# Kernel tuning notes

Measured on AMD Instinct MI355X. Metric: run time of the kernel, lower is better.

## Reference

```python
import jax, jax.numpy as jnp
import numpy as np

B, IN_LEN, NN, IN_DIM = 32, 28, 2048, 1
E, ND = 256, 256          # embed_dim, node_dim
H = E + ND                # hidden_dim = 512
N_LAYERS = 3
OUT_LEN = 28


def setup_inputs() -> dict:
    key = jax.random.key(0)
    ks = jax.random.split(key, 16)
    x_node = jax.random.normal(ks[0], (B, IN_LEN, NN, IN_DIM), jnp.float32)
    # x_state channels: [0]=cumulative cases, [1]=infected I, [2]=population N
    col0 = jax.random.uniform(ks[1], (B, IN_LEN, NN, 1), jnp.float32) * 100.0
    colI = jax.random.uniform(ks[2], (B, IN_LEN, NN, 1), jnp.float32) * 100.0 + 1.0
    colN = 1e4 * (1.0 + 0.1 * jax.random.uniform(ks[3], (B, IN_LEN, NN, 1), jnp.float32))
    x_state = jnp.concatenate([col0, colI, colN], axis=-1)
    node_emb = jax.random.normal(ks[4], (NN, ND), jnp.float32) * 0.05
    W_ts = jax.random.normal(ks[5], (E, IN_DIM * IN_LEN), jnp.float32) * 0.05
    b_ts = jnp.zeros((E,), jnp.float32)
    enc_W1 = jax.random.normal(ks[6], (N_LAYERS, H, H), jnp.float32) * 0.02
    enc_b1 = jnp.zeros((N_LAYERS, H), jnp.float32)
    enc_W2 = jax.random.normal(ks[7], (N_LAYERS, H, H), jnp.float32) * 0.02
    enc_b2 = jnp.zeros((N_LAYERS, H), jnp.float32)
    Wb = jax.random.normal(ks[8], (1, H), jnp.float32) * 0.05
    bb = jnp.zeros((1,), jnp.float32)
    Wg = jax.random.normal(ks[9], (1, H), jnp.float32) * 0.05
    bg = jnp.zeros((1,), jnp.float32)
    return dict(x_node=x_node, x_state=x_state, node_emb=node_emb,
                W_ts=W_ts, b_ts=b_ts, enc_W1=enc_W1, enc_b1=enc_b1,
                enc_W2=enc_W2, enc_b2=enc_b2, Wb=Wb, bb=bb, Wg=Wg, bg=bg)


def _forward(x_node, x_state, node_emb, W_ts, b_ts,
             enc_W1, enc_b1, enc_W2, enc_b2, Wb, bb, Wg, bg):
    Bn, Lh, Nn, _ = x_node.shape
    # [B,L,N,D] -> [B,N,L*D] (channel = in_dim*in_len for 1x1 conv == linear)
    flat = jnp.transpose(x_node[..., :IN_DIM], (0, 2, 1, 3)).reshape(Bn, Nn, Lh * IN_DIM)
    ts = flat @ W_ts.T + b_ts                                  # [B,N,E]
    h = jnp.concatenate(
        [ts, jnp.broadcast_to(node_emb[None], (Bn,) + node_emb.shape)], axis=-1)  # [B,N,H]
    for l in range(enc_W1.shape[0]):                            # residual MLP encoder
        z = jnp.maximum(h @ enc_W1[l].T + enc_b1[l], 0.0)
        h = h + z @ enc_W2[l].T + enc_b2[l]
    b = jax.nn.sigmoid(h @ Wb.T + bb)                           # [B,N,1] infection rate
    g = jax.nn.sigmoid(h @ Wg.T + bg)                           # [B,N,1] recovery rate

    Npop = x_state[:, -1, :, 2:3]                               # [B,N,1]
    I_hist = x_state[..., 1:2] / g[:, None]                     # [B,L,N,1]
    Iin_hist = jnp.maximum(
        I_hist[:, 1:] - I_hist[:, :-1] + x_state[:, :-1, :, 1:2], 0.0)  # [B,L-1,N,1]
    t1 = jnp.arange(Lh - 1, 0, -1, dtype=jnp.float32)
    w1 = jnp.exp(-g[:, None] * t1[None, :, None, None])         # [B,L-1,N,1]
    I_Tm1 = jnp.sum(w1 * Iin_hist, axis=1)                      # [B,N,1]
    R_Tm1 = Npop - x_state[:, -2, :, 0:1]
    S_Tm1 = Npop - I_Tm1 - R_Tm1
    Iin0 = b * S_Tm1 * I_Tm1 / Npop
    Rin0 = g * I_hist[:, -1, :, 0:1]
    Iin_hist = jnp.concatenate([Iin_hist, Iin0[:, None]], axis=1)  # [B,L,N,1]
    S = S_Tm1 - Iin0
    t2 = jnp.arange(Lh, 0, -1, dtype=jnp.float32)
    w2 = jnp.exp(-g[:, None] * t2[None, :, None, None])
    I = jnp.sum(w2 * Iin_hist, axis=1)                          # [B,N,1]
    R = R_Tm1 + Rin0

    # The torch loop recomputes sum_i exp(-g*(L-i))*Iin_i each step; exact identity:
    # I_new = exp(-g) * (I_old + Iin_new). O(T) scan instead of O(T^2).
    decay = jnp.exp(-g)

    def step(carry, _):
        S, I, R = carry
        Iin = b * S * I / Npop
        S = S - Iin
        Rin = g * I            # uses pre-update I_T, matching torch order
        I = decay * (I + Iin)
        R = R + Rin
        return (S, I, R), Rin

    _, rins = jax.lax.scan(step, (S, I, R), None, length=OUT_LEN)  # [T,B,N,1]
    return jnp.transpose(rins, (1, 0, 2, 3))                       # [B,out_len,N,1]


def reference(x_node, x_state, node_emb, W_ts, b_ts, enc_W1, enc_b1,
              enc_W2, enc_b2, Wb, bb, Wg, bg):
    return _forward(x_node, x_state, node_emb, W_ts, b_ts,
                    enc_W1, enc_b1, enc_W2, enc_b2, Wb, bb, Wg, bg)
```

## Files before the change

kernel.cpp:

```cpp
#include <hip/hip_runtime.h>
#include <hip/hip_bf16.h>
#include <math.h>

#define BATCH 32
#define IN_LEN 28
#define NN 2048
#define E 256
#define H 512
#define N_LAYERS 3
#define OUT_LEN 28
#define M_ROWS (BATCH * NN)

typedef unsigned short u16;
typedef unsigned int   u32;
typedef __attribute__((ext_vector_type(8))) short short8;
typedef __attribute__((ext_vector_type(4))) float f32x4;

__device__ __forceinline__ u16 f2h(float x) {
    union { _Float16 h; u16 u; } v; v.h = (_Float16)x; return v.u;
}
__device__ __forceinline__ float h2f(u16 u) {
    union { _Float16 h; u16 u; } v; v.u = u; return (float)v.h;
}

__device__ __forceinline__ void gload_lds16(const void* g, void* l) {
    __builtin_amdgcn_global_load_lds(
        (const __attribute__((address_space(1))) void*)g,
        (__attribute__((address_space(3))) void*)l, 16, 0, 0);
}

__global__ __launch_bounds__(256)
void k_split2(const float* __restrict__ w1, const float* __restrict__ w2,
              u16* __restrict__ hi, u16* __restrict__ lo, int nW)
{
    int i = blockIdx.x * 256 + threadIdx.x;
    float v = (i < nW) ? w1[i] : w2[i - nW];
    u16 h = f2h(v);
    hi[i] = h;
    lo[i] = f2h(v - h2f(h));
}

__global__ __launch_bounds__(256)
void k_ts(const float* __restrict__ x_node, const float* __restrict__ node_emb,
          const float* __restrict__ W_ts, const float* __restrict__ b_ts,
          u16* __restrict__ hhi, u16* __restrict__ hlo)
{
    __shared__ float xs[IN_LEN][64];
    const int tid = threadIdx.x;
    const int b   = blockIdx.y;
    const int n0  = blockIdx.x * 64;

    for (int idx = tid; idx < IN_LEN * 64; idx += 256) {
        int l = idx >> 6, i = idx & 63;
        xs[l][i] = x_node[((size_t)b * IN_LEN + l) * NN + n0 + i];
    }
    __syncthreads();

    float w[IN_LEN];
    #pragma unroll
    for (int j = 0; j < IN_LEN; j++) w[j] = W_ts[tid * IN_LEN + j];
    const float bias = b_ts[tid];

    for (int i = 0; i < 64; i++) {
        float acc = bias;
        #pragma unroll
        for (int j = 0; j < IN_LEN; j++) acc += xs[j][i] * w[j];
        size_t row = (size_t)b * NN + n0 + i;
        u16 thi = f2h(acc);
        hhi[row * H + tid] = thi;
        hlo[row * H + tid] = f2h(acc - h2f(thi));
        float ev = node_emb[(size_t)(n0 + i) * 256 + tid];
        u16 ehi = f2h(ev);
        hhi[row * H + E + tid] = ehi;
        hlo[row * H + E + tid] = f2h(ev - h2f(ehi));
    }
}

__global__ __launch_bounds__(256)
void k_gemm1(const u16* __restrict__ Ahi, const u16* __restrict__ Alo,
             const u16* __restrict__ Whi, const u16* __restrict__ Wlo,
             const float* __restrict__ bias, u16* __restrict__ Z)
{
    __shared__ __align__(16) u16 smem[32768];

    const int tid = threadIdx.x;
    const int ln  = tid & 63;
    const int wv  = tid >> 6;

    const int id   = blockIdx.x;
    const int c    = (id >> 3) & 3;
    const int r    = (id & 7) | ((id >> 5) << 3);
    const int row0 = r * 128;
    const int col0 = c * 128;

    const int rbase = (wv & 1) * 64;
    const int cbase = (wv >> 1) * 64;

    const int lr = ln >> 2;
    const int lc = ln & 3;

    const u16* sgsrc; int sofs; int tb;
    if      (wv == 0) { sgsrc = Ahi; sofs = 0;     tb = row0; }
    else if (wv == 1) { sgsrc = Alo; sofs = 8192;  tb = row0; }
    else if (wv == 2) { sgsrc = Whi; sofs = 16384; tb = col0; }
    else              { sgsrc = Wlo; sofs = 24576; tb = col0; }

    auto stage = [&](int p, int kt) {
        u16* dstbuf = smem + sofs + p * 4096;
        #pragma unroll
        for (int i = 0; i < 8; i++) {
            int row = i * 16 + lr;
            int sc  = lc ^ ((row >> 1) & 3);
            gload_lds16(sgsrc + (size_t)(tb + row) * H + kt + sc * 8,
                        dstbuf + i * 512);
        }
    };

    f32x4 acc[4][4];
    #pragma unroll
    for (int m = 0; m < 4; m++)
        #pragma unroll
        for (int n = 0; n < 4; n++) acc[m][n] = (f32x4)(0.f);

    stage(0, 0);

    const int wl = ln & 15;

    for (int t = 0; t < 16; t++) {
        const int p = t & 1;
        __syncthreads();
        if (t + 1 < 16) stage(1 - p, (t + 1) * 32);

        const u16* bAh = smem + 0     + p * 4096;
        const u16* bAl = smem + 8192  + p * 4096;
        const u16* bWh = smem + 16384 + p * 4096;
        const u16* bWl = smem + 24576 + p * 4096;

        short8 ahi[4], alo[4], whi[4], wlo[4];
        #pragma unroll
        for (int m = 0; m < 4; m++) {
            int rr = rbase + m * 16 + wl;
            int cc = ((ln >> 4) ^ ((rr >> 1) & 3)) * 8;
            ahi[m] = *(const short8*)&bAh[rr * 32 + cc];
            alo[m] = *(const short8*)&bAl[rr * 32 + cc];
        }
        #pragma unroll
        for (int n = 0; n < 4; n++) {
            int wr = cbase + n * 16 + wl;
            int cc = ((ln >> 4) ^ ((wr >> 1) & 3)) * 8;
            whi[n] = *(const short8*)&bWh[wr * 32 + cc];
            wlo[n] = *(const short8*)&bWl[wr * 32 + cc];
        }
        #pragma unroll
        for (int m = 0; m < 4; m++)
            #pragma unroll
            for (int n = 0; n < 4; n++) {
                acc[m][n] = __builtin_amdgcn_mfma_f32_16x16x32_f16(ahi[m], whi[n], acc[m][n], 0, 0, 0);
                acc[m][n] = __builtin_amdgcn_mfma_f32_16x16x32_f16(ahi[m], wlo[n], acc[m][n], 0, 0, 0);
                acc[m][n] = __builtin_amdgcn_mfma_f32_16x16x32_f16(alo[m], whi[n], acc[m][n], 0, 0, 0);
            }
    }

    __syncthreads();
    u16* zb = smem + wv * 4096;
    float bv[4];
    #pragma unroll
    for (int n = 0; n < 4; n++) bv[n] = bias[col0 + cbase + n * 16 + wl];
    #pragma unroll
    for (int m = 0; m < 4; m++)
        #pragma unroll
        for (int n = 0; n < 4; n++)
            #pragma unroll
            for (int rg = 0; rg < 4; rg++) {
                int row_l = m * 16 + (ln >> 4) * 4 + rg;
                zb[row_l * 64 + n * 16 + wl] =
                    f2h(fmaxf(acc[m][n][rg] + bv[n], 0.f));
            }
    const int cr = ln >> 3;
    const int cc = (ln & 7) * 8;
    #pragma unroll
    for (int p2 = 0; p2 < 8; p2++) {
        int row_l = cr + p2 * 8;
        uint4 v = *(const uint4*)&zb[row_l * 64 + cc];
        *(uint4*)&Z[(size_t)(row0 + rbase + row_l) * H + col0 + cbase + cc] = v;
    }
}

__global__ __launch_bounds__(256)
void k_gemm2(const u16* __restrict__ Z,
             const u16* __restrict__ Whi, const u16* __restrict__ Wlo,
             const float* __restrict__ bias,
             u16* HHi, u16* HLo)
{
    __shared__ __align__(16) u16 smem[24576];

    const int tid = threadIdx.x;
    const int ln  = tid & 63;
    const int wv  = tid >> 6;

    const int id   = blockIdx.x;
    const int c    = (id >> 3) & 3;
    const int r    = (id & 7) | ((id >> 5) << 3);
    const int row0 = r * 128;
    const int col0 = c * 128;

    const int rbase = (wv & 1) * 64;
    const int cbase = (wv >> 1) * 64;

    const int lr = ln >> 2;
    const int lc = ln & 3;

    const u16* sgsrc; int sofs; int tb; int iofs; int niss;
    if      (wv == 0) { sgsrc = Z;   sofs = 0;     tb = row0;      iofs = 0;    niss = 4; }
    else if (wv == 3) { sgsrc = Z;   sofs = 0;     tb = row0 + 64; iofs = 2048; niss = 4; }
    else if (wv == 1) { sgsrc = Whi; sofs = 8192;  tb = col0;      iofs = 0;    niss = 8; }
    else              { sgsrc = Wlo; sofs = 16384; tb = col0;      iofs = 0;    niss = 8; }

    auto stage = [&](int p, int kt) {
        u16* dstbuf = smem + sofs + p * 4096 + iofs;
        #pragma unroll
        for (int i = 0; i < 8; i++) {
            if (i >= niss) break;
            int row = i * 16 + lr;
            int sc  = lc ^ ((row >> 1) & 3);
            gload_lds16(sgsrc + (size_t)(tb + row) * H + kt + sc * 8,
                        dstbuf + i * 512);
        }
    };

    stage(0, 0);

    const int cr  = ln >> 3;
    const int ccl = (ln & 7) * 4;
    uint2 resh[2][8], resl[2][8];
    #pragma unroll
    for (int nh = 0; nh < 2; nh++) {
        const int gc0 = col0 + cbase + nh * 32 + ccl;
        #pragma unroll
        for (int p2 = 0; p2 < 8; p2++) {
            size_t gidx = (size_t)(row0 + rbase + cr + p2 * 8) * H + gc0;
            resh[nh][p2] = *(const uint2*)(HHi + gidx);
            resl[nh][p2] = *(const uint2*)(HLo + gidx);
        }
    }

    f32x4 acc[4][4];
    #pragma unroll
    for (int m = 0; m < 4; m++)
        #pragma unroll
        for (int n = 0; n < 4; n++) acc[m][n] = (f32x4)(0.f);

    const int wl = ln & 15;

    for (int t = 0; t < 16; t++) {
        const int p = t & 1;
        __syncthreads();
        if (t + 1 < 16) stage(1 - p, (t + 1) * 32);

        const u16* bZ  = smem + 0     + p * 4096;
        const u16* bWh = smem + 8192  + p * 4096;
        const u16* bWl = smem + 16384 + p * 4096;

        short8 az[4], whi[4], wlo[4];
        #pragma unroll
        for (int m = 0; m < 4; m++) {
            int rr = rbase + m * 16 + wl;
            int cc = ((ln >> 4) ^ ((rr >> 1) & 3)) * 8;
            az[m] = *(const short8*)&bZ[rr * 32 + cc];
        }
        #pragma unroll
        for (int n = 0; n < 4; n++) {
            int wr = cbase + n * 16 + wl;
            int cc = ((ln >> 4) ^ ((wr >> 1) & 3)) * 8;
            whi[n] = *(const short8*)&bWh[wr * 32 + cc];
            wlo[n] = *(const short8*)&bWl[wr * 32 + cc];
        }
        #pragma unroll
        for (int m = 0; m < 4; m++)
            #pragma unroll
            for (int n = 0; n < 4; n++) {
                acc[m][n] = __builtin_amdgcn_mfma_f32_16x16x32_f16(az[m], whi[n], acc[m][n], 0, 0, 0);
                acc[m][n] = __builtin_amdgcn_mfma_f32_16x16x32_f16(az[m], wlo[n], acc[m][n], 0, 0, 0);
            }
    }

    __syncthreads();
    float* fb = (float*)smem + wv * 2048;

    #pragma unroll
    for (int nh = 0; nh < 2; nh++) {
        #pragma unroll
        for (int m = 0; m < 4; m++)
            #pragma unroll
            for (int j = 0; j < 2; j++)
                #pragma unroll
                for (int rg = 0; rg < 4; rg++) {
                    int row_l = m * 16 + (ln >> 4) * 4 + rg;
                    fb[row_l * 32 + j * 16 + wl] = acc[m][nh * 2 + j][rg];
                }
        const int gc0 = col0 + cbase + nh * 32 + ccl;
        float4 bv = *(const float4*)&bias[gc0];
        #pragma unroll
        for (int p2 = 0; p2 < 8; p2++) {
            int row_l = cr + p2 * 8;
            size_t gidx = (size_t)(row0 + rbase + row_l) * H + gc0;
            uint2 uh = resh[nh][p2];
            uint2 ul = resl[nh][p2];
            float4 a = *(const float4*)&fb[row_l * 32 + ccl];
            float v0 = a.x + bv.x + h2f((u16)(uh.x & 0xFFFF)) + h2f((u16)(ul.x & 0xFFFF));
            float v1 = a.y + bv.y + h2f((u16)(uh.x >> 16))    + h2f((u16)(ul.x >> 16));
            float v2 = a.z + bv.z + h2f((u16)(uh.y & 0xFFFF)) + h2f((u16)(ul.y & 0xFFFF));
            float v3 = a.w + bv.w + h2f((u16)(uh.y >> 16))    + h2f((u16)(ul.y >> 16));
            u16 h0 = f2h(v0), h1 = f2h(v1), h2 = f2h(v2), h3 = f2h(v3);
            uint2 oh, ol;
            oh.x = (u32)h0 | ((u32)h1 << 16);
            oh.y = (u32)h2 | ((u32)h3 << 16);
            ol.x = (u32)f2h(v0 - h2f(h0)) | ((u32)f2h(v1 - h2f(h1)) << 16);
            ol.y = (u32)f2h(v2 - h2f(h2)) | ((u32)f2h(v3 - h2f(h3)) << 16);
            *(uint2*)(HHi + gidx) = oh;
            *(uint2*)(HLo + gidx) = ol;
        }
    }
}

__global__ __launch_bounds__(256)
void k_head(const u16* __restrict__ hhi, const u16* __restrict__ hlo,
            const float* __restrict__ Wb, const float* __restrict__ bb,
            const float* __restrict__ Wg, const float* __restrict__ bg,
            float* __restrict__ bArr, float* __restrict__ gArr)
{
    const int lane = threadIdx.x & 63;
    const int row  = blockIdx.x * 4 + (threadIdx.x >> 6);

    uint4 uh = *(const uint4*)(hhi + (size_t)row * H + lane * 8);
    uint4 ul = *(const uint4*)(hlo + (size_t)row * H + lane * 8);
    u32 ph[4] = {uh.x, uh.y, uh.z, uh.w};
    u32 pl[4] = {ul.x, ul.y, ul.z, ul.w};
    float hv[8];
    #pragma unroll
    for (int k = 0; k < 4; k++) {
        hv[2 * k]     = h2f((u16)(ph[k] & 0xFFFF)) + h2f((u16)(pl[k] & 0xFFFF));
        hv[2 * k + 1] = h2f((u16)(ph[k] >> 16))    + h2f((u16)(pl[k] >> 16));
    }
    float4 wb0 = *(const float4*)(Wb + lane * 8);
    float4 wb1 = *(const float4*)(Wb + lane * 8 + 4);
    float4 wg0 = *(const float4*)(Wg + lane * 8);
    float4 wg1 = *(const float4*)(Wg + lane * 8 + 4);

    float sb = hv[0] * wb0.x + hv[1] * wb0.y + hv[2] * wb0.z + hv[3] * wb0.w
             + hv[4] * wb1.x + hv[5] * wb1.y + hv[6] * wb1.z + hv[7] * wb1.w;
    float sg = hv[0] * wg0.x + hv[1] * wg0.y + hv[2] * wg0.z + hv[3] * wg0.w
             + hv[4] * wg1.x + hv[5] * wg1.y + hv[6] * wg1.z + hv[7] * wg1.w;

    #pragma unroll
    for (int off = 32; off >= 1; off >>= 1) {
        sb += __shfl_xor(sb, off);
        sg += __shfl_xor(sg, off);
    }
    if (lane == 0) {
        bArr[row] = 1.f / (1.f + expf(-(sb + bb[0])));
        gArr[row] = 1.f / (1.f + expf(-(sg + bg[0])));
    }
}

__global__ __launch_bounds__(256)
void k_sir(const float* __restrict__ x_state,
           const float* __restrict__ bArr, const float* __restrict__ gArr,
           float* __restrict__ out)
{
    const int row = blockIdx.x * 256 + threadIdx.x;
    const int bb_ = row / NN;
    const int n   = row % NN;

    const float g = gArr[row];
    const float b = bArr[row];
    const float d = expf(-g);

    const float* xs = x_state + ((size_t)bb_ * IN_LEN) * (NN * 3) + (size_t)n * 3;

    float x1_prev = xs[1];
    float Ih_prev = x1_prev / g;
    float acc = 0.f;
    #pragma unroll 4
    for (int t = 1; t <= IN_LEN - 1; ++t) {
        float x1 = xs[(size_t)t * (NN * 3) + 1];
        float Ih = x1 / g;
        float Iin = fmaxf(Ih - Ih_prev + x1_prev, 0.f);
        acc = acc * d + Iin;
        Ih_prev = Ih;
        x1_prev = x1;
    }
    float ITm1 = acc * d;
    float Npop = xs[(size_t)(IN_LEN - 1) * (NN * 3) + 2];
    float RTm1 = Npop - xs[(size_t)(IN_LEN - 2) * (NN * 3) + 0];
    float STm1 = Npop - ITm1 - RTm1;
    float Iin0 = b * STm1 * ITm1 / Npop;
    float S = STm1 - Iin0;
    float I = d * (ITm1 + Iin0);

    float* op = out + ((size_t)bb_ * OUT_LEN) * NN + n;
    #pragma unroll 4
    for (int k = 0; k < OUT_LEN; k++) {
        float Iin = b * S * I / Npop;
        S = S - Iin;
        float Rin = g * I;
        I = d * (I + Iin);
        op[(size_t)k * NN] = Rin;
    }
}

extern "C" void kernel_launch(void* const* d_in, const int* in_sizes, int n_in,
                              void* d_out, int out_size, void* d_ws, size_t ws_size,
                              hipStream_t stream)
{
    const float* x_node   = (const float*)d_in[0];
    const float* x_state  = (const float*)d_in[1];
    const float* node_emb = (const float*)d_in[2];
    const float* W_ts     = (const float*)d_in[3];
    const float* b_ts     = (const float*)d_in[4];
    const float* enc_W1   = (const float*)d_in[5];
    const float* enc_b1   = (const float*)d_in[6];
    const float* enc_W2   = (const float*)d_in[7];
    const float* enc_b2   = (const float*)d_in[8];
    const float* Wb       = (const float*)d_in[9];
    const float* bb       = (const float*)d_in[10];
    const float* Wg       = (const float*)d_in[11];
    const float* bg       = (const float*)d_in[12];
    float* out = (float*)d_out;

    u16* hhi   = (u16*)d_ws;
    u16* hlo   = hhi + (size_t)M_ROWS * H;
    u16* wHi   = hlo + (size_t)M_ROWS * H;
    u16* wLo   = wHi + (size_t)6 * H * H;
    float* bArr = (float*)(wLo + (size_t)6 * H * H);
    float* gArr = bArr + M_ROWS;
    u16* z     = (u16*)(gArr + M_ROWS);

    size_t used  = (size_t)((char*)z - (char*)d_ws);
    size_t avail = (ws_size > used) ? ws_size - used : 0;
    long long chunkLL = (long long)(avail / (H * sizeof(u16))) & ~1023LL;
    int chunk = (chunkLL > M_ROWS) ? M_ROWS : (int)chunkLL;
    if (chunk < 1024) chunk = 1024;

    const int nW = N_LAYERS * H * H;
    k_split2<<<2 * nW / 256, 256, 0, stream>>>(enc_W1, enc_W2, wHi, wLo, nW);

    k_ts<<<dim3(NN / 64, BATCH), 256, 0, stream>>>(x_node, node_emb, W_ts, b_ts, hhi, hlo);

    for (int l = 0; l < N_LAYERS; l++) {
        const u16* W1hi = wHi + (size_t)l * H * H;
        const u16* W1lo = wLo + (size_t)l * H * H;
        const u16* W2hi = wHi + (size_t)nW + (size_t)l * H * H;
        const u16* W2lo = wLo + (size_t)nW + (size_t)l * H * H;
        const float* b1 = enc_b1 + (size_t)l * H;
        const float* b2 = enc_b2 + (size_t)l * H;
        for (int r = 0; r < M_ROWS; r += chunk) {
            int rows = (M_ROWS - r < chunk) ? (M_ROWS - r) : chunk;
            u16* hrhi = hhi + (size_t)r * H;
            u16* hrlo = hlo + (size_t)r * H;
            int nblk = (rows / 128) * 4;
            k_gemm1<<<nblk, 256, 0, stream>>>(hrhi, hrlo, W1hi, W1lo, b1, z);
            k_gemm2<<<nblk, 256, 0, stream>>>(z, W2hi, W2lo, b2, hrhi, hrlo);
        }
    }

    k_head<<<M_ROWS / 4, 256, 0, stream>>>(hhi, hlo, Wb, bb, Wg, bg, bArr, gArr);

    k_sir<<<M_ROWS / 256, 256, 0, stream>>>(x_state, bArr, gArr, out);
}
```

Measured before the change: 853.8 us.

## Fuse beta/gamma head projection into last-layer GEMM2 epilogue with atomics

Removes the separate k_head kernel. The last encoder layer's GEMM2 epilogue now computes partial dot products with Wb and Wg, reduces them across 8 lanes, and atomically adds them into per-row sums. The sigmoid moves into k_sir. The residual loads of H are also moved from before the K loop into the epilogue, which lowers register pressure during the MFMA loop but exposes that load latency at the end. This saves a full re-read of the hidden state, at the cost of a memset, atomics across 4 column blocks, and order-dependent float summation.

Measured after the change: 787.5 us. 7.8% less time.

```diff
diff --git a/kernel.cpp b/kernel.cpp
--- a/kernel.cpp
+++ b/kernel.cpp
@@ -186,11 +186,14 @@
     }
 }
 
+template <int HEAD>
 __global__ __launch_bounds__(256)
 void k_gemm2(const u16* __restrict__ Z,
              const u16* __restrict__ Whi, const u16* __restrict__ Wlo,
              const float* __restrict__ bias,
-             u16* HHi, u16* HLo)
+             u16* HHi, u16* HLo,
+             const float* __restrict__ Wb, const float* __restrict__ Wg,
+             float* __restrict__ bSum, float* __restrict__ gSum)
 {
     __shared__ __align__(16) u16 smem[24576];
 
@@ -228,27 +231,13 @@
         }
     };
 
+    f32x4 acc[4][4];
+    #pragma unroll
+    for (int m = 0; m < 4; m++)
+        #pragma unroll
+        for (int n = 0; n < 4; n++) acc[m][n] = (f32x4)(0.f);
+
     stage(0, 0);
-
-    const int cr  = ln >> 3;
-    const int ccl = (ln & 7) * 4;
-    uint2 resh[2][8], resl[2][8];
-    #pragma unroll
-    for (int nh = 0; nh < 2; nh++) {
-        const int gc0 = col0 + cbase + nh * 32 + ccl;
-        #pragma unroll
-        for (int p2 = 0; p2 < 8; p2++) {
-            size_t gidx = (size_t)(row0 + rbase + cr + p2 * 8) * H + gc0;
-            resh[nh][p2] = *(const uint2*)(HHi + gidx);
-            resl[nh][p2] = *(const uint2*)(HLo + gidx);
-        }
-    }
-
-    f32x4 acc[4][4];
-    #pragma unroll
-    for (int m = 0; m < 4; m++)
-        #pragma unroll
-        for (int n = 0; n < 4; n++) acc[m][n] = (f32x4)(0.f);
 
     const int wl = ln & 15;
 
@@ -286,6 +275,14 @@
 
     __syncthreads();
     float* fb = (float*)smem + wv * 2048;
+
+    const int cr  = ln >> 3;
+    const int ccl = (ln & 7) * 4;
+    float pb[8], pg[8];
+    if (HEAD) {
+        #pragma unroll
+        for (int p2 = 0; p2 < 8; p2++) { pb[p2] = 0.f; pg[p2] = 0.f; }
+    }
 
     #pragma unroll
     for (int nh = 0; nh < 2; nh++) {
@@ -300,17 +297,26 @@
                 }
         const int gc0 = col0 + cbase + nh * 32 + ccl;
         float4 bv = *(const float4*)&bias[gc0];
+        float4 hb, hg;
+        if (HEAD) {
+            hb = *(const float4*)&Wb[gc0];
+            hg = *(const float4*)&Wg[gc0];
+        }
         #pragma unroll
         for (int p2 = 0; p2 < 8; p2++) {
             int row_l = cr + p2 * 8;
             size_t gidx = (size_t)(row0 + rbase + row_l) * H + gc0;
-            uint2 uh = resh[nh][p2];
-            uint2 ul = resl[nh][p2];
+            uint2 uh = *(const uint2*)(HHi + gidx);
+            uint2 ul = *(const uint2*)(HLo + gidx);
             float4 a = *(const float4*)&fb[row_l * 32 + ccl];
             float v0 = a.x + bv.x + h2f((u16)(uh.x & 0xFFFF)) + h2f((u16)(ul.x & 0xFFFF));
             float v1 = a.y + bv.y + h2f((u16)(uh.x >> 16))    + h2f((u16)(ul.x >> 16));
             float v2 = a.z + bv.z + h2f((u16)(uh.y & 0xFFFF)) + h2f((u16)(ul.y & 0xFFFF));
             float v3 = a.w + bv.w + h2f((u16)(uh.y >> 16))    + h2f((u16)(ul.y >> 16));
+            if (HEAD) {
+                pb[p2] += v0 * hb.x + v1 * hb.y + v2 * hb.z + v3 * hb.w;
+                pg[p2] += v0 * hg.x + v1 * hg.y + v2 * hg.z + v3 * hg.w;
+            }
             u16 h0 = f2h(v0), h1 = f2h(v1), h2 = f2h(v2), h3 = f2h(v3);
             uint2 oh, ol;
             oh.x = (u32)h0 | ((u32)h1 << 16);
@@ -321,59 +327,37 @@
             *(uint2*)(HLo + gidx) = ol;
         }
     }
-}
-
-__global__ __launch_bounds__(256)
-void k_head(const u16* __restrict__ hhi, const u16* __restrict__ hlo,
-            const float* __restrict__ Wb, const float* __restrict__ bb,
-            const float* __restrict__ Wg, const float* __restrict__ bg,
-            float* __restrict__ bArr, float* __restrict__ gArr)
-{
-    const int lane = threadIdx.x & 63;
-    const int row  = blockIdx.x * 4 + (threadIdx.x >> 6);
-
-    uint4 uh = *(const uint4*)(hhi + (size_t)row * H + lane * 8);
-    uint4 ul = *(const uint4*)(hlo + (size_t)row * H + lane * 8);
-    u32 ph[4] = {uh.x, uh.y, uh.z, uh.w};
-    u32 pl[4] = {ul.x, ul.y, ul.z, ul.w};
-    float hv[8];
-    #pragma unroll
-    for (int k = 0; k < 4; k++) {
-        hv[2 * k]     = h2f((u16)(ph[k] & 0xFFFF)) + h2f((u16)(pl[k] & 0xFFFF));
-        hv[2 * k + 1] = h2f((u16)(ph[k] >> 16))    + h2f((u16)(pl[k] >> 16));
-    }
-    float4 wb0 = *(const float4*)(Wb + lane * 8);
-    float4 wb1 = *(const float4*)(Wb + lane * 8 + 4);
-    float4 wg0 = *(const float4*)(Wg + lane * 8);
-    float4 wg1 = *(const float4*)(Wg + lane * 8 + 4);
-
-    float sb = hv[0] * wb0.x + hv[1] * wb0.y + hv[2] * wb0.z + hv[3] * wb0.w
-             + hv[4] * wb1.x + hv[5] * wb1.y + hv[6] * wb1.z + hv[7] * wb1.w;
-    float sg = hv[0] * wg0.x + hv[1] * wg0.y + hv[2] * wg0.z + hv[3] * wg0.w
-             + hv[4] * wg1.x + hv[5] * wg1.y + hv[6] * wg1.z + hv[7] * wg1.w;
-
-    #pragma unroll
-    for (int off = 32; off >= 1; off >>= 1) {
-        sb += __shfl_xor(sb, off);
-        sg += __shfl_xor(sg, off);
-    }
-    if (lane == 0) {
-        bArr[row] = 1.f / (1.f + expf(-(sb + bb[0])));
-        gArr[row] = 1.f / (1.f + expf(-(sg + bg[0])));
+
+    if (HEAD) {
+        #pragma unroll
+        for (int p2 = 0; p2 < 8; p2++) {
+            float sb = pb[p2], sg = pg[p2];
+            #pragma unroll
+            for (int off = 1; off < 8; off <<= 1) {
+                sb += __shfl_xor(sb, off);
+                sg += __shfl_xor(sg, off);
+            }
+            if ((ln & 7) == 0) {
+                int grow = row0 + rbase + cr + p2 * 8;
+                atomicAdd(&bSum[grow], sb);
+                atomicAdd(&gSum[grow], sg);
+            }
+        }
     }
 }
 
 __global__ __launch_bounds__(256)
 void k_sir(const float* __restrict__ x_state,
-           const float* __restrict__ bArr, const float* __restrict__ gArr,
+           const float* __restrict__ bSum, const float* __restrict__ gSum,
+           const float* __restrict__ bb, const float* __restrict__ bg,
            float* __restrict__ out)
 {
     const int row = blockIdx.x * 256 + threadIdx.x;
     const int bb_ = row / NN;
     const int n   = row % NN;
 
-    const float g = gArr[row];
-    const float b = bArr[row];
+    const float g = 1.f / (1.f + expf(-(gSum[row] + bg[0])));
+    const float b = 1.f / (1.f + expf(-(bSum[row] + bb[0])));
     const float d = expf(-g);
 
     const float* xs = x_state + ((size_t)bb_ * IN_LEN) * (NN * 3) + (size_t)n * 3;
@@ -432,15 +416,17 @@
     u16* hlo   = hhi + (size_t)M_ROWS * H;
     u16* wHi   = hlo + (size_t)M_ROWS * H;
     u16* wLo   = wHi + (size_t)6 * H * H;
-    float* bArr = (float*)(wLo + (size_t)6 * H * H);
-    float* gArr = bArr + M_ROWS;
-    u16* z     = (u16*)(gArr + M_ROWS);
+    float* bSum = (float*)(wLo + (size_t)6 * H * H);
+    float* gSum = bSum + M_ROWS;
+    u16* z     = (u16*)(gSum + M_ROWS);
 
     size_t used  = (size_t)((char*)z - (char*)d_ws);
     size_t avail = (ws_size > used) ? ws_size - used : 0;
     long long chunkLL = (long long)(avail / (H * sizeof(u16))) & ~1023LL;
     int chunk = (chunkLL > M_ROWS) ? M_ROWS : (int)chunkLL;
     if (chunk < 1024) chunk = 1024;
+
+    hipMemsetAsync(bSum, 0, 2 * (size_t)M_ROWS * sizeof(float), stream);
 
     const int nW = N_LAYERS * H * H;
     k_split2<<<2 * nW / 256, 256, 0, stream>>>(enc_W1, enc_W2, wHi, wLo, nW);
@@ -460,11 +446,14 @@
             u16* hrlo = hlo + (size_t)r * H;
             int nblk = (rows / 128) * 4;
             k_gemm1<<<nblk, 256, 0, stream>>>(hrhi, hrlo, W1hi, W1lo, b1, z);
-            k_gemm2<<<nblk, 256, 0, stream>>>(z, W2hi, W2lo, b2, hrhi, hrlo);
-        }
-    }
-
-    k_head<<<M_ROWS / 4, 256, 0, stream>>>(hhi, hlo, Wb, bb, Wg, bg, bArr, gArr);
-
-    k_sir<<<M_ROWS / 256, 256, 0, stream>>>(x_state, bArr, gArr, out);
-}
+            if (l < N_LAYERS - 1)
+                k_gemm2<0><<<nblk, 256, 0, stream>>>(z, W2hi, W2lo, b2, hrhi, hrlo,
+                                                     Wb, Wg, bSum, gSum);
+            else
+                k_gemm2<1><<<nblk, 256, 0, stream>>>(z, W2hi, W2lo, b2, hrhi, hrlo,
+                                                     Wb, Wg, bSum, gSum);
+        }
+    }
+
+    k_sir<<<M_ROWS / 256, 256, 0, stream>>>(x_state, bSum, gSum, bb, bg, out);
+}
```
